# Performance work log

Hardware: AMD Instinct MI355X
Metric: run time of the kernel (lower is better)

Reference implementation:

```python
import jax, jax.numpy as jnp
import numpy as np

T, B, D, A = 512, 64, 1024, 128
NL = 2
AIN = A + 2 * D        # adapt LSTM input size: adapt + x + alstm hidden
PSZ = 2 * D + 12 * D   # policy size per layer (bias=True): ninp+nhid + 12*nhid


def setup_inputs() -> dict:
    key = jax.random.key(0)
    ks = jax.random.split(key, 12)
    r = lambda k, s: jax.random.normal(k, s, dtype=jnp.float32) * 0.03
    return {
        "x": jax.random.normal(ks[0], (T, B, D), dtype=jnp.float32),
        # layer 0
        "a_wih0": r(ks[1], (4 * A, AIN)), "a_whh0": r(ks[2], (4 * A, A)),
        "a_bih0": jnp.zeros((4 * A,), jnp.float32), "a_bhh0": jnp.zeros((4 * A,), jnp.float32),
        "p_w0": r(ks[3], (PSZ, A)), "p_b0": jnp.ones((PSZ,), jnp.float32),
        "f_wih0": r(ks[4], (4 * D, D)), "f_whh0": r(ks[5], (4 * D, D)),
        "f_b0": jnp.zeros((4 * D,), jnp.float32),
        # layer 1
        "a_wih1": r(ks[6], (4 * A, AIN)), "a_whh1": r(ks[7], (4 * A, A)),
        "a_bih1": jnp.zeros((4 * A,), jnp.float32), "a_bhh1": jnp.zeros((4 * A,), jnp.float32),
        "p_w1": r(ks[8], (PSZ, A)), "p_b1": jnp.ones((PSZ,), jnp.float32),
        "f_wih1": r(ks[9], (4 * D, D)), "f_whh1": r(ks[10], (4 * D, D)),
        "f_b1": jnp.zeros((4 * D,), jnp.float32),
    }


def _lstm_cell(x, h, c, wih, whh, bih, bhh):
    g = x @ wih.T + bih + h @ whh.T + bhh      # [B, 4A]
    i, f, gg, o = jnp.split(g, 4, axis=1)
    c2 = jax.nn.sigmoid(f) * c + jax.nn.sigmoid(i) * jnp.tanh(gg)
    h2 = jax.nn.sigmoid(o) * jnp.tanh(c2)
    return h2, c2


def _alstm_cell(xt, h, c, pol, wih, whh, b):
    # policy chunks: [ninp, nhid, 4n, 4n, 4n] with ninp=nhid=D
    p0 = pol[:, :D]
    p1 = pol[:, D:2 * D]
    p2 = pol[:, 2 * D:6 * D]
    p3 = pol[:, 6 * D:10 * D]
    p4 = pol[:, 10 * D:14 * D]
    ig = ((xt * p0) @ wih.T) * p2 + b * p4
    hg = ((h * p1) @ whh.T) * p3
    g = ig + hg
    i, f, gg, o = jnp.split(g, 4, axis=1)
    c2 = jax.nn.sigmoid(f) * c + jax.nn.sigmoid(i) * jnp.tanh(gg)
    h2 = jax.nn.sigmoid(o) * jnp.tanh(c2)
    return h2, c2


def reference(x, a_wih0, a_whh0, a_bih0, a_bhh0, p_w0, p_b0, f_wih0, f_whh0, f_b0,
              a_wih1, a_whh1, a_bih1, a_bhh1, p_w1, p_b1, f_wih1, f_whh1, f_b1):
    params = [
        (a_wih0, a_whh0, a_bih0, a_bhh0, p_w0, p_b0, f_wih0, f_whh0, f_b0),
        (a_wih1, a_whh1, a_bih1, a_bhh1, p_w1, p_b1, f_wih1, f_whh1, f_b1),
    ]

    def step(carry, xt):
        ah, ac, fh, fc = (list(t) for t in carry)
        xc = xt
        for l in range(NL):
            awih, awhh, abih, abhh, pw, pb, fwih, fwhh, fb = params[l]
            # nlayers != 1: adapt input = [x, alstm hidden, prev-layer adapt hidden]
            # (Python negative indexing at l=0 picks last layer's adapt hidden from t-1,
            #  matching the torch in-place list update semantics.)
            ax = jnp.concatenate([xc, fh[l], ah[l - 1]], axis=1)
            ah[l], ac[l] = _lstm_cell(ax, ah[l], ac[l], awih, awhh, abih, abhh)
            pol = ah[l] @ pw.T + pb                      # Project: Linear(A -> PSZ)
            fh[l], fc[l] = _alstm_cell(xc, fh[l], fc[l], pol, fwih, fwhh, fb)
            xc = fh[l]
        return (tuple(ah), tuple(ac), tuple(fh), tuple(fc)), xc

    za = jnp.zeros((B, A), x.dtype)
    zf = jnp.zeros((B, D), x.dtype)
    carry0 = ((za,) * NL, (za,) * NL, (zf,) * NL, (zf,) * NL)
    _, ys = jax.lax.scan(step, carry0, x)   # [T, B, D]
    return ys
```

## Files before the change

kernel.cpp:

```cpp
#include <hip/hip_runtime.h>

#define T_ 512
#define B_ 64
#define D_ 1024
#define A_ 128
#define KCAT_ 2304
#define PSZ_ 14336
#define NBLK 224

typedef __attribute__((ext_vector_type(8))) short short8;
typedef __attribute__((ext_vector_type(4))) short short4_t;
typedef __attribute__((ext_vector_type(4))) float float4_t;
typedef __attribute__((ext_vector_type(2))) unsigned long long ull2;

__device__ __forceinline__ float sigf(float x){ return 1.0f/(1.0f + __expf(-x)); }
__device__ __forceinline__ float tanhf_(float x){ return 2.0f/(1.0f + __expf(-2.0f*x)) - 1.0f; }

__device__ __forceinline__ short f2bf(float f){
  unsigned u = __builtin_bit_cast(unsigned, f);
  u += 0x7fffu + ((u >> 16) & 1u);
  return (short)(u >> 16);
}
__device__ __forceinline__ float bf2f(short s){
  unsigned u = ((unsigned)(unsigned short)s) << 16;
  return __builtin_bit_cast(float, u);
}

__device__ __forceinline__ unsigned ld_u32_cg(const void* p){
  return __hip_atomic_load((const unsigned*)p, __ATOMIC_RELAXED, __HIP_MEMORY_SCOPE_AGENT);
}
__device__ __forceinline__ unsigned long long ld_u64_cg(const void* p){
  return __hip_atomic_load((const unsigned long long*)p, __ATOMIC_RELAXED, __HIP_MEMORY_SCOPE_AGENT);
}
__device__ __forceinline__ void st_u32_cg(void* p, unsigned v){
  __hip_atomic_store((unsigned*)p, v, __ATOMIC_RELAXED, __HIP_MEMORY_SCOPE_AGENT);
}
__device__ __forceinline__ void st_u64_cg(void* p, unsigned long long v){
  __hip_atomic_store((unsigned long long*)p, v, __ATOMIC_RELAXED, __HIP_MEMORY_SCOPE_AGENT);
}
__device__ __forceinline__ float ld_f_cg(const float* p){
  unsigned u = ld_u32_cg(p); return __builtin_bit_cast(float, u);
}
__device__ __forceinline__ void st_f_cg(float* p, float v){
  st_u32_cg(p, __builtin_bit_cast(unsigned, v));
}
__device__ __forceinline__ short8 ld_bf8_cg(const short* p){
  ull2 t; t.x = ld_u64_cg(p); t.y = ld_u64_cg(p + 4);
  return __builtin_bit_cast(short8, t);
}
__device__ __forceinline__ short4_t ld_bf4_cg(const short* p){
  return __builtin_bit_cast(short4_t, ld_u64_cg(p));
}
__device__ __forceinline__ float4_t ld_f4_cg(const float* p){
  ull2 t; t.x = ld_u64_cg(p); t.y = ld_u64_cg(p + 2);
  return __builtin_bit_cast(float4_t, t);
}
__device__ __forceinline__ void st_bf4_cg(short* p, short4_t v){
  st_u64_cg(p, __builtin_bit_cast(unsigned long long, v));
}
__device__ __forceinline__ void st_f4_cg(float* p, float4_t v){
  ull2 t = __builtin_bit_cast(ull2, v);
  st_u64_cg(p, t.x); st_u64_cg(p + 2, t.y);
}

__global__ __launch_bounds__(256) void pk_cat(const float* __restrict__ wih,
                                              const float* __restrict__ whh,
                                              short* __restrict__ dst){
  int c = blockIdx.x*256 + threadIdx.x;
  int n = blockIdx.y;
  if (c >= KCAT_) return;
  float v = (c < 2176) ? wih[(size_t)n*2176 + c] : whh[n*A_ + (c - 2176)];
  dst[(size_t)n*KCAT_ + c] = f2bf(v);
}
__global__ __launch_bounds__(256) void pk_conv(const float* __restrict__ src,
                                               short* __restrict__ dst, int n){
  int i = blockIdx.x*256 + threadIdx.x;
  if (i < n) dst[i] = f2bf(src[i]);
}

struct Args {
  const float* x;
  const short* Wcat0; const short* Wcat1;
  const float* bih0;  const float* bih1;
  const float* bhh0;  const float* bhh1;
  const short* pw0;   const short* pw1;
  const float* pb0;   const float* pb1;
  const short* fwi0;  const short* fwi1;
  const short* fwh0;  const short* fwh1;
  const float* fb0;   const float* fb1;
  float* gates; float* ac; float* fc; float* polp;
  short* xp0; short* hp1; short* fhbf; short* ahbf;
  float* out;
  unsigned* bar;
};

__device__ __forceinline__ void gsync(unsigned* bar, unsigned target){
  __syncthreads();
  if (threadIdx.x == 0){
    __hip_atomic_fetch_add(bar, 1u, __ATOMIC_RELAXED, __HIP_MEMORY_SCOPE_AGENT);
    while (__hip_atomic_load(bar, __ATOMIC_RELAXED, __HIP_MEMORY_SCOPE_AGENT) < target)
      __builtin_amdgcn_s_sleep(2);
  }
  __syncthreads();
}

__global__ __launch_bounds__(256, 1) void fused(Args P){
  const int tid  = threadIdx.x;
  const int blk  = blockIdx.x;
  const int wq   = tid >> 6;
  const int lane = tid & 63;
  const int row  = lane & 15, quad = lane >> 4;

  __shared__ float red[4][256];
  __shared__ short ah_s[64*136];

  unsigned ph = 0;

  for (int t = 0; t < T_; ++t){
    const int par = t & 1, cur = par ^ 1;
    const float* xt = P.x + (size_t)t*B_*D_;
    #pragma unroll
    for (int l = 0; l < 2; ++l){
      const short* Wcat = l ? P.Wcat1 : P.Wcat0;
      const float* bih  = l ? P.bih1  : P.bih0;
      const float* bhh  = l ? P.bhh1  : P.bhh0;
      const short* pw   = l ? P.pw1   : P.pw0;
      const float* pb   = l ? P.pb1   : P.pb0;
      const short* fwi  = l ? P.fwi1  : P.fwi0;
      const short* fwh  = l ? P.fwh1  : P.fwh0;
      const float* fb   = l ? P.fb1   : P.fb0;
      short* fh_l = P.fhbf + (size_t)l*B_*D_;
      const short* ahp = l ? (P.ahbf + (0*2 + cur)*B_*A_)
                           : (P.ahbf + (1*2 + par)*B_*A_);
      const short* ahs = P.ahbf + (l*2 + par)*B_*A_;
      short* ah_out    = P.ahbf + (l*2 + cur)*B_*A_;
      const float* ac_old = P.ac + (l*2 + par)*A_*B_;
      float* ac_new       = P.ac + (l*2 + cur)*A_*B_;
      float* fc_l = P.fc + (size_t)l*B_*D_;

      if (blk < 128){
        const int m0  = (blk >> 2) * 16;
        const int nt1 = blk & 3;
        const int bq  = nt1*16 + row;
        const short* wrow = Wcat + (size_t)(m0 + row)*KCAT_ + quad*8;
        float4_t acc = {0.f,0.f,0.f,0.f};
        if (l == 0){
          const float* xp = xt + (size_t)bq*D_ + quad*8;
          #pragma unroll
          for (int i = 0; i < 8; ++i){
            const int ks = wq + 4*i;
            short8 a = *(const short8*)(wrow + ks*32);
            float4_t x0 = *(const float4_t*)(xp + ks*32);
            float4_t x1 = *(const float4_t*)(xp + ks*32 + 4);
            short8 bfr;
            #pragma unroll
            for (int r = 0; r < 4; ++r){ bfr[r] = f2bf(x0[r]); bfr[4+r] = f2bf(x1[r]); }
            acc = __builtin_amdgcn_mfma_f32_16x16x32_bf16(a, bfr, acc, 0, 0, 0);
          }
        } else {
          const short* xp = P.fhbf + (size_t)bq*D_;
          #pragma unroll
          for (int i = 0; i < 8; ++i){
            const int ks = wq + 4*i;
            short8 a = *(const short8*)(wrow + ks*32);
            short8 bfr = ld_bf8_cg(xp + quad*8 + ks*32);
            acc = __builtin_amdgcn_mfma_f32_16x16x32_bf16(a, bfr, acc, 0, 0, 0);
          }
        }
        {
          const short* hp = fh_l + (size_t)bq*D_;
          #pragma unroll
          for (int i = 0; i < 8; ++i){
            const int ks = wq + 4*i;
            short8 a = *(const short8*)(wrow + 1024 + ks*32);
            short8 bfr = ld_bf8_cg(hp + quad*8 + ks*32);
            acc = __builtin_amdgcn_mfma_f32_16x16x32_bf16(a, bfr, acc, 0, 0, 0);
          }
        }
        {
          short8 a = *(const short8*)(wrow + 2048 + wq*32);
          short8 bfr = ld_bf8_cg(ahp + bq*A_ + quad*8 + wq*32);
          acc = __builtin_amdgcn_mfma_f32_16x16x32_bf16(a, bfr, acc, 0, 0, 0);
        }
        {
          short8 a = *(const short8*)(wrow + 2176 + wq*32);
          short8 bfr = ld_bf8_cg(ahs + bq*A_ + quad*8 + wq*32);
          acc = __builtin_amdgcn_mfma_f32_16x16x32_bf16(a, bfr, acc, 0, 0, 0);
        }
        #pragma unroll
        for (int r = 0; r < 4; ++r) red[wq][(r << 6) | lane] = acc[r];
        __syncthreads();
        {
          float s = red[0][tid] + red[1][tid] + red[2][tid] + red[3][tid];
          const int rr = tid >> 6, ll = tid & 63;
          const int n = m0 + ((ll >> 4) << 2) + rr;
          const int b = nt1*16 + (ll & 15);
          st_f_cg(&P.gates[n*B_ + b], s + bih[n] + bhh[n]);
        }
      }
      gsync(P.bar, ++ph * NBLK);

      {
        const int b = tid & 63, q = tid >> 6;
        unsigned long long pk = 0;
        #pragma unroll 8
        for (int jj = 0; jj < 32; ++jj){
          const int j = q*32 + jj;
          float gi = ld_f_cg(&P.gates[(j      )*B_ + b]);
          float gf = ld_f_cg(&P.gates[(j + 128)*B_ + b]);
          float gg = ld_f_cg(&P.gates[(j + 256)*B_ + b]);
          float go = ld_f_cg(&P.gates[(j + 384)*B_ + b]);
          float c  = ld_f_cg(&ac_old[j*B_ + b]);
          float c2 = sigf(gf)*c + sigf(gi)*tanhf_(gg);
          float h2 = sigf(go)*tanhf_(c2);
          short hb = f2bf(h2);
          ah_s[b*136 + j] = hb;
          if (blk == 0){
            st_f_cg(&ac_new[j*B_ + b], c2);
            pk |= (unsigned long long)(unsigned short)hb << ((jj & 3)*16);
            if ((jj & 3) == 3){ st_u64_cg(ah_out + b*A_ + (j - 3), pk); pk = 0; }
          }
        }
        __syncthreads();
        const int m0 = (blk*4 + wq)*16;
        const short* wrow = pw + (size_t)(m0 + row)*A_ + quad*8;
        float4_t acc[4] = {{0.f,0.f,0.f,0.f},{0.f,0.f,0.f,0.f},{0.f,0.f,0.f,0.f},{0.f,0.f,0.f,0.f}};
        #pragma unroll
        for (int ks = 0; ks < 4; ++ks){
          short8 a = *(const short8*)(wrow + ks*32);
          #pragma unroll
          for (int nt = 0; nt < 4; ++nt){
            short8 bf8 = *(const short8*)&ah_s[(nt*16 + row)*136 + ks*32 + quad*8];
            acc[nt] = __builtin_amdgcn_mfma_f32_16x16x32_bf16(a, bf8, acc[nt], 0, 0, 0);
          }
        }
        const int c0 = m0 + quad*4;
        float4_t pbv = *(const float4_t*)(pb + c0);
        if (m0 < 1024){
          #pragma unroll
          for (int nt = 0; nt < 4; ++nt){
            const int b2 = nt*16 + row;
            float4_t xv;
            if (l == 0){ xv = *(const float4_t*)(xt + (size_t)b2*D_ + c0); }
            else {
              short4_t xb = ld_bf4_cg(P.fhbf + (size_t)b2*D_ + c0);
              #pragma unroll
              for (int r = 0; r < 4; ++r) xv[r] = bf2f(xb[r]);
            }
            short4_t o;
            #pragma unroll
            for (int r = 0; r < 4; ++r) o[r] = f2bf((acc[nt][r] + pbv[r]) * xv[r]);
            st_bf4_cg(P.xp0 + (size_t)b2*D_ + c0, o);
          }
        } else if (m0 < 2048){
          const int cc = c0 - 1024;
          #pragma unroll
          for (int nt = 0; nt < 4; ++nt){
            const int b2 = nt*16 + row;
            short4_t hb = ld_bf4_cg(fh_l + (size_t)b2*D_ + cc);
            short4_t o;
            #pragma unroll
            for (int r = 0; r < 4; ++r) o[r] = f2bf((acc[nt][r] + pbv[r]) * bf2f(hb[r]));
            st_bf4_cg(P.hp1 + (size_t)b2*D_ + cc, o);
          }
        } else {
          const int cc = c0 - 2048;
          #pragma unroll
          for (int nt = 0; nt < 4; ++nt){
            const int b2 = nt*16 + row;
            float4_t vv;
            #pragma unroll
            for (int r = 0; r < 4; ++r) vv[r] = acc[nt][r] + pbv[r];
            st_f4_cg(P.polp + (size_t)b2*12288 + cc, vv);
          }
        }
      }
      gsync(P.bar, ++ph * NBLK);

      if (blk < 64){
        const int nt3 = wq;
        const int j0 = blk*16;
        const short* wIr[4]; const short* wHr[4];
        #pragma unroll
        for (int g = 0; g < 4; ++g){
          wIr[g] = fwi + (size_t)(g*D_ + j0 + row)*D_ + quad*8;
          wHr[g] = fwh + (size_t)(g*D_ + j0 + row)*D_ + quad*8;
        }
        const short* bx = P.xp0 + (size_t)(nt3*16 + row)*D_ + quad*8;
        const short* bh = P.hp1 + (size_t)(nt3*16 + row)*D_ + quad*8;
        float4_t aI[4] = {{0.f,0.f,0.f,0.f},{0.f,0.f,0.f,0.f},{0.f,0.f,0.f,0.f},{0.f,0.f,0.f,0.f}};
        float4_t aH[4] = {{0.f,0.f,0.f,0.f},{0.f,0.f,0.f,0.f},{0.f,0.f,0.f,0.f},{0.f,0.f,0.f,0.f}};
        #pragma unroll 2
        for (int ks = 0; ks < 32; ++ks){
          const int kg = ks*32;
          short8 bxf = ld_bf8_cg(bx + kg);
          short8 bhf = ld_bf8_cg(bh + kg);
          #pragma unroll
          for (int g = 0; g < 4; ++g){
            short8 ai  = *(const short8*)(wIr[g] + kg);
            short8 ah8 = *(const short8*)(wHr[g] + kg);
            aI[g] = __builtin_amdgcn_mfma_f32_16x16x32_bf16(ai,  bxf, aI[g], 0, 0, 0);
            aH[g] = __builtin_amdgcn_mfma_f32_16x16x32_bf16(ah8, bhf, aH[g], 0, 0, 0);
          }
        }
        const int b3 = nt3*16 + row;
        const int jr = j0 + quad*4;
        float4_t gl[4];
        #pragma unroll
        for (int g = 0; g < 4; ++g){
          const float* pbase = P.polp + (size_t)b3*12288 + g*D_ + jr;
          float4_t p2 = ld_f4_cg(pbase);
          float4_t p3 = ld_f4_cg(pbase + 4096);
          float4_t p4 = ld_f4_cg(pbase + 8192);
          float4_t fbv = *(const float4_t*)(fb + g*D_ + jr);
          #pragma unroll
          for (int r = 0; r < 4; ++r)
            gl[g][r] = aI[g][r]*p2[r] + fbv[r]*p4[r] + aH[g][r]*p3[r];
        }
        float4_t cold = *(const float4_t*)(fc_l + (size_t)b3*D_ + jr);
        float4_t cnew, hnew;
        #pragma unroll
        for (int r = 0; r < 4; ++r){
          float c2 = sigf(gl[1][r])*cold[r] + sigf(gl[0][r])*tanhf_(gl[2][r]);
          float h2 = sigf(gl[3][r])*tanhf_(c2);
          cnew[r] = c2; hnew[r] = h2;
        }
        *(float4_t*)(fc_l + (size_t)b3*D_ + jr) = cnew;
        short4_t hb;
        #pragma unroll
        for (int r = 0; r < 4; ++r) hb[r] = f2bf(hnew[r]);
        st_bf4_cg(fh_l + (size_t)b3*D_ + jr, hb);
        if (l == 1)
          __builtin_nontemporal_store(hnew,
              (float4_t*)(P.out + (size_t)t*B_*D_ + (size_t)b3*D_ + jr));
      }
      gsync(P.bar, ++ph * NBLK);
    }
  }
}

extern "C" void kernel_launch(void* const* d_in, const int* in_sizes, int n_in,
                              void* d_out, int out_size, void* d_ws, size_t ws_size,
                              hipStream_t stream) {
  const float* x = (const float*)d_in[0];
  const float* a_wih[2] = {(const float*)d_in[1],  (const float*)d_in[10]};
  const float* a_whh[2] = {(const float*)d_in[2],  (const float*)d_in[11]};
  const float* a_bih[2] = {(const float*)d_in[3],  (const float*)d_in[12]};
  const float* a_bhh[2] = {(const float*)d_in[4],  (const float*)d_in[13]};
  const float* p_w[2]   = {(const float*)d_in[5],  (const float*)d_in[14]};
  const float* p_b[2]   = {(const float*)d_in[6],  (const float*)d_in[15]};
  const float* f_wih[2] = {(const float*)d_in[7],  (const float*)d_in[16]};
  const float* f_whh[2] = {(const float*)d_in[8],  (const float*)d_in[17]};
  const float* f_b[2]   = {(const float*)d_in[9],  (const float*)d_in[18]};

  char* w = (char*)d_ws;
  float* gates = (float*)(w + 0);
  float* ac    = (float*)(w + 131072);
  float* fc    = (float*)(w + 262144);
  float* polp  = (float*)(w + 786432);
  short* xp0   = (short*)(w + 3932160);
  short* hp1   = (short*)(w + 4063232);
  short* fhbf  = (short*)(w + 4194304);
  short* ahbf  = (short*)(w + 4456448);
  short* Wcat  = (short*)(w + 4521984);
  short* pwbf  = (short*)(w + 9240576);
  short* fwihb = (short*)(w + 16580608);
  short* fwhhb = (short*)(w + 33357824);
  unsigned* bar = (unsigned*)(w + 50135040);

  hipMemsetAsync(w + 131072, 0, 655360, stream);
  hipMemsetAsync(w + 4194304, 0, 327680, stream);
  hipMemsetAsync(w + 50135040, 0, 64, stream);

  for (int l = 0; l < 2; ++l){
    pk_cat<<<dim3(9,512), 256, 0, stream>>>(a_wih[l], a_whh[l], Wcat + (size_t)l*512*KCAT_);
    pk_conv<<<(PSZ_*A_ + 255)/256, 256, 0, stream>>>(p_w[l], pwbf + (size_t)l*PSZ_*A_, PSZ_*A_);
    pk_conv<<<(4*D_*D_ + 255)/256, 256, 0, stream>>>(f_wih[l], fwihb + (size_t)l*4*D_*D_, 4*D_*D_);
    pk_conv<<<(4*D_*D_ + 255)/256, 256, 0, stream>>>(f_whh[l], fwhhb + (size_t)l*4*D_*D_, 4*D_*D_);
  }

  Args A;
  A.x = x;
  A.Wcat0 = Wcat;  A.Wcat1 = Wcat + (size_t)512*KCAT_;
  A.bih0 = a_bih[0]; A.bih1 = a_bih[1];
  A.bhh0 = a_bhh[0]; A.bhh1 = a_bhh[1];
  A.pw0 = pwbf;    A.pw1 = pwbf + (size_t)PSZ_*A_;
  A.pb0 = p_b[0];  A.pb1 = p_b[1];
  A.fwi0 = fwihb;  A.fwi1 = fwihb + (size_t)4*D_*D_;
  A.fwh0 = fwhhb;  A.fwh1 = fwhhb + (size_t)4*D_*D_;
  A.fb0 = f_b[0];  A.fb1 = f_b[1];
  A.gates = gates; A.ac = ac; A.fc = fc; A.polp = polp;
  A.xp0 = xp0; A.hp1 = hp1; A.fhbf = fhbf; A.ahbf = ahbf;
  A.out = (float*)d_out;
  A.bar = bar;

  fused<<<NBLK, 256, 0, stream>>>(A);
}
```

Before: 96.72 ms.

## Keep ALSTM weights resident in LDS across all timesteps with flag-based grid barrier

The persistent kernel now uses 256 blocks. Each block converts its slice of the adaptive-LSTM input and hidden weights to bf16 once and keeps them in shared memory for the whole sequence, so it no longer streams them from global memory every step. Each layer's gate GEMM runs on the 128 blocks that own that layer's slice, with a lane shuffle to combine the gates. The atomic-counter barrier becomes per-block flags that every block polls, and the small adapt-LSTM GEMM moves to 32 blocks with no cross-wave reduction. In exchange, half the blocks sit idle in the ALSTM phase of each layer, and about 132KB of LDS per block limits occupancy to one block per CU.

```diff
diff --git a/kernel.cpp b/kernel.cpp
--- a/kernel.cpp
+++ b/kernel.cpp
@@ -6,7 +6,8 @@
 #define A_ 128
 #define KCAT_ 2304
 #define PSZ_ 14336
-#define NBLK 224
+#define NBLK 256
+#define RS_ 1032
 
 typedef __attribute__((ext_vector_type(8))) short short8;
 typedef __attribute__((ext_vector_type(4))) short short4_t;
@@ -85,24 +86,14 @@
   const float* bhh0;  const float* bhh1;
   const short* pw0;   const short* pw1;
   const float* pb0;   const float* pb1;
-  const short* fwi0;  const short* fwi1;
-  const short* fwh0;  const short* fwh1;
+  const float* fwi32_0; const float* fwi32_1;
+  const float* fwh32_0; const float* fwh32_1;
   const float* fb0;   const float* fb1;
   float* gates; float* ac; float* fc; float* polp;
   short* xp0; short* hp1; short* fhbf; short* ahbf;
   float* out;
-  unsigned* bar;
+  unsigned* flags;
 };
-
-__device__ __forceinline__ void gsync(unsigned* bar, unsigned target){
-  __syncthreads();
-  if (threadIdx.x == 0){
-    __hip_atomic_fetch_add(bar, 1u, __ATOMIC_RELAXED, __HIP_MEMORY_SCOPE_AGENT);
-    while (__hip_atomic_load(bar, __ATOMIC_RELAXED, __HIP_MEMORY_SCOPE_AGENT) < target)
-      __builtin_amdgcn_s_sleep(2);
-  }
-  __syncthreads();
-}
 
 __global__ __launch_bounds__(256, 1) void fused(Args P){
   const int tid  = threadIdx.x;
@@ -111,8 +102,28 @@
   const int lane = tid & 63;
   const int row  = lane & 15, quad = lane >> 4;
 
-  __shared__ float red[4][256];
+  __shared__ short wlds[2][32][RS_];
   __shared__ short ah_s[64*136];
+
+  {
+    const int l3 = blk >> 7, jt = blk & 127;
+    const float* srcI = l3 ? P.fwi32_1 : P.fwi32_0;
+    const float* srcH = l3 ? P.fwh32_1 : P.fwh32_0;
+    for (int e = tid; e < 8192; e += 256){
+      const int rr = e >> 8;
+      const int k4 = (e & 255) << 2;
+      const int g = rr >> 3, r = rr & 7;
+      const size_t off = ((size_t)(g*1024 + jt*8 + r))*1024 + k4;
+      float4_t vI = *(const float4_t*)(srcI + off);
+      float4_t vH = *(const float4_t*)(srcH + off);
+      short4_t oI, oH;
+      #pragma unroll
+      for (int j = 0; j < 4; ++j){ oI[j] = f2bf(vI[j]); oH[j] = f2bf(vH[j]); }
+      *(short4_t*)&wlds[0][rr][k4] = oI;
+      *(short4_t*)&wlds[1][rr][k4] = oH;
+    }
+    __syncthreads();
+  }
 
   unsigned ph = 0;
 
@@ -126,8 +137,6 @@
       const float* bhh  = l ? P.bhh1  : P.bhh0;
       const short* pw   = l ? P.pw1   : P.pw0;
       const float* pb   = l ? P.pb1   : P.pb0;
-      const short* fwi  = l ? P.fwi1  : P.fwi0;
-      const short* fwh  = l ? P.fwh1  : P.fwh0;
       const float* fb   = l ? P.fb1   : P.fb0;
       short* fh_l = P.fhbf + (size_t)l*B_*D_;
       const short* ahp = l ? (P.ahbf + (0*2 + cur)*B_*A_)
@@ -138,17 +147,15 @@
       float* ac_new       = P.ac + (l*2 + cur)*A_*B_;
       float* fc_l = P.fc + (size_t)l*B_*D_;
 
-      if (blk < 128){
-        const int m0  = (blk >> 2) * 16;
-        const int nt1 = blk & 3;
-        const int bq  = nt1*16 + row;
+      if (blk < 32){
+        const int m0 = blk*16;
+        const int bq = wq*16 + row;
         const short* wrow = Wcat + (size_t)(m0 + row)*KCAT_ + quad*8;
         float4_t acc = {0.f,0.f,0.f,0.f};
         if (l == 0){
           const float* xp = xt + (size_t)bq*D_ + quad*8;
-          #pragma unroll
-          for (int i = 0; i < 8; ++i){
-            const int ks = wq + 4*i;
+          #pragma unroll 4
+          for (int ks = 0; ks < 32; ++ks){
             short8 a = *(const short8*)(wrow + ks*32);
             float4_t x0 = *(const float4_t*)(xp + ks*32);
             float4_t x1 = *(const float4_t*)(xp + ks*32 + 4);
@@ -158,49 +165,53 @@
             acc = __builtin_amdgcn_mfma_f32_16x16x32_bf16(a, bfr, acc, 0, 0, 0);
           }
         } else {
-          const short* xp = P.fhbf + (size_t)bq*D_;
-          #pragma unroll
-          for (int i = 0; i < 8; ++i){
-            const int ks = wq + 4*i;
+          const short* xp = P.fhbf + (size_t)bq*D_ + quad*8;
+          #pragma unroll 4
+          for (int ks = 0; ks < 32; ++ks){
             short8 a = *(const short8*)(wrow + ks*32);
-            short8 bfr = ld_bf8_cg(xp + quad*8 + ks*32);
+            short8 bfr = ld_bf8_cg(xp + ks*32);
             acc = __builtin_amdgcn_mfma_f32_16x16x32_bf16(a, bfr, acc, 0, 0, 0);
           }
         }
         {
-          const short* hp = fh_l + (size_t)bq*D_;
-          #pragma unroll
-          for (int i = 0; i < 8; ++i){
-            const int ks = wq + 4*i;
+          const short* hp = fh_l + (size_t)bq*D_ + quad*8;
+          #pragma unroll 4
+          for (int ks = 0; ks < 32; ++ks){
             short8 a = *(const short8*)(wrow + 1024 + ks*32);
-            short8 bfr = ld_bf8_cg(hp + quad*8 + ks*32);
+            short8 bfr = ld_bf8_cg(hp + ks*32);
             acc = __builtin_amdgcn_mfma_f32_16x16x32_bf16(a, bfr, acc, 0, 0, 0);
           }
         }
-        {
-          short8 a = *(const short8*)(wrow + 2048 + wq*32);
-          short8 bfr = ld_bf8_cg(ahp + bq*A_ + quad*8 + wq*32);
+        #pragma unroll
+        for (int ks = 0; ks < 4; ++ks){
+          short8 a = *(const short8*)(wrow + 2048 + ks*32);
+          short8 bfr = ld_bf8_cg(ahp + bq*A_ + quad*8 + ks*32);
           acc = __builtin_amdgcn_mfma_f32_16x16x32_bf16(a, bfr, acc, 0, 0, 0);
         }
-        {
-          short8 a = *(const short8*)(wrow + 2176 + wq*32);
-          short8 bfr = ld_bf8_cg(ahs + bq*A_ + quad*8 + wq*32);
+        #pragma unroll
+        for (int ks = 0; ks < 4; ++ks){
+          short8 a = *(const short8*)(wrow + 2176 + ks*32);
+          short8 bfr = ld_bf8_cg(ahs + bq*A_ + quad*8 + ks*32);
           acc = __builtin_amdgcn_mfma_f32_16x16x32_bf16(a, bfr, acc, 0, 0, 0);
         }
         #pragma unroll
-        for (int r = 0; r < 4; ++r) red[wq][(r << 6) | lane] = acc[r];
+        for (int r = 0; r < 4; ++r){
+          const int n = m0 + quad*4 + r;
+          st_f_cg(&P.gates[n*B_ + bq], acc[r] + bih[n] + bhh[n]);
+        }
+      }
+      {
+        ++ph;
         __syncthreads();
-        {
-          float s = red[0][tid] + red[1][tid] + red[2][tid] + red[3][tid];
-          const int rr = tid >> 6, ll = tid & 63;
-          const int n = m0 + ((ll >> 4) << 2) + rr;
-          const int b = nt1*16 + (ll & 15);
-          st_f_cg(&P.gates[n*B_ + b], s + bih[n] + bhh[n]);
-        }
-      }
-      gsync(P.bar, ++ph * NBLK);
-
-      {
+        if (tid == 0) st_u32_cg(P.flags + blk*16, ph);
+        for (;;){
+          int bad = (ld_u32_cg(P.flags + tid*16) < ph);
+          if (__syncthreads_count(bad) == 0) break;
+          __builtin_amdgcn_s_sleep(1);
+        }
+      }
+
+      if (blk < 224){
         const int b = tid & 63, q = tid >> 6;
         unsigned long long pk = 0;
         #pragma unroll 8
@@ -275,66 +286,87 @@
           }
         }
       }
-      gsync(P.bar, ++ph * NBLK);
-
-      if (blk < 64){
-        const int nt3 = wq;
-        const int j0 = blk*16;
-        const short* wIr[4]; const short* wHr[4];
-        #pragma unroll
-        for (int g = 0; g < 4; ++g){
-          wIr[g] = fwi + (size_t)(g*D_ + j0 + row)*D_ + quad*8;
-          wHr[g] = fwh + (size_t)(g*D_ + j0 + row)*D_ + quad*8;
-        }
-        const short* bx = P.xp0 + (size_t)(nt3*16 + row)*D_ + quad*8;
-        const short* bh = P.hp1 + (size_t)(nt3*16 + row)*D_ + quad*8;
-        float4_t aI[4] = {{0.f,0.f,0.f,0.f},{0.f,0.f,0.f,0.f},{0.f,0.f,0.f,0.f},{0.f,0.f,0.f,0.f}};
-        float4_t aH[4] = {{0.f,0.f,0.f,0.f},{0.f,0.f,0.f,0.f},{0.f,0.f,0.f,0.f},{0.f,0.f,0.f,0.f}};
+      {
+        ++ph;
+        __syncthreads();
+        if (tid == 0) st_u32_cg(P.flags + blk*16, ph);
+        for (;;){
+          int bad = (ld_u32_cg(P.flags + tid*16) < ph);
+          if (__syncthreads_count(bad) == 0) break;
+          __builtin_amdgcn_s_sleep(1);
+        }
+      }
+
+      if ((blk >> 7) == l){
+        const int jt = blk & 127;
+        const int b  = wq*16 + row;
+        const short* bx = P.xp0 + (size_t)b*D_ + quad*8;
+        const short* bh = P.hp1 + (size_t)b*D_ + quad*8;
+        float4_t aI[2] = {{0.f,0.f,0.f,0.f},{0.f,0.f,0.f,0.f}};
+        float4_t aH[2] = {{0.f,0.f,0.f,0.f},{0.f,0.f,0.f,0.f}};
         #pragma unroll 2
         for (int ks = 0; ks < 32; ++ks){
-          const int kg = ks*32;
-          short8 bxf = ld_bf8_cg(bx + kg);
-          short8 bhf = ld_bf8_cg(bh + kg);
-          #pragma unroll
-          for (int g = 0; g < 4; ++g){
-            short8 ai  = *(const short8*)(wIr[g] + kg);
-            short8 ah8 = *(const short8*)(wHr[g] + kg);
-            aI[g] = __builtin_amdgcn_mfma_f32_16x16x32_bf16(ai,  bxf, aI[g], 0, 0, 0);
-            aH[g] = __builtin_amdgcn_mfma_f32_16x16x32_bf16(ah8, bhf, aH[g], 0, 0, 0);
-          }
-        }
-        const int b3 = nt3*16 + row;
-        const int jr = j0 + quad*4;
-        float4_t gl[4];
-        #pragma unroll
-        for (int g = 0; g < 4; ++g){
-          const float* pbase = P.polp + (size_t)b3*12288 + g*D_ + jr;
+          short8 bxf = ld_bf8_cg(bx + ks*32);
+          short8 bhf = ld_bf8_cg(bh + ks*32);
+          #pragma unroll
+          for (int tp = 0; tp < 2; ++tp){
+            short8 aIf = *(const short8*)&wlds[0][tp*16 + row][quad*8 + ks*32];
+            short8 aHf = *(const short8*)&wlds[1][tp*16 + row][quad*8 + ks*32];
+            aI[tp] = __builtin_amdgcn_mfma_f32_16x16x32_bf16(aIf, bxf, aI[tp], 0, 0, 0);
+            aH[tp] = __builtin_amdgcn_mfma_f32_16x16x32_bf16(aHf, bhf, aH[tp], 0, 0, 0);
+          }
+        }
+        const int g0 = quad >> 1;
+        const int jb = (quad & 1) * 4;
+        const int jg = jt*8 + jb;
+        float gl[2][4];
+        #pragma unroll
+        for (int tp = 0; tp < 2; ++tp){
+          const int g = tp*2 + g0;
+          const float* pbase = P.polp + (size_t)b*12288 + g*1024 + jg;
           float4_t p2 = ld_f4_cg(pbase);
           float4_t p3 = ld_f4_cg(pbase + 4096);
           float4_t p4 = ld_f4_cg(pbase + 8192);
-          float4_t fbv = *(const float4_t*)(fb + g*D_ + jr);
+          float4_t fbv = *(const float4_t*)(fb + g*1024 + jg);
           #pragma unroll
           for (int r = 0; r < 4; ++r)
-            gl[g][r] = aI[g][r]*p2[r] + fbv[r]*p4[r] + aH[g][r]*p3[r];
-        }
-        float4_t cold = *(const float4_t*)(fc_l + (size_t)b3*D_ + jr);
-        float4_t cnew, hnew;
-        #pragma unroll
-        for (int r = 0; r < 4; ++r){
-          float c2 = sigf(gl[1][r])*cold[r] + sigf(gl[0][r])*tanhf_(gl[2][r]);
-          float h2 = sigf(gl[3][r])*tanhf_(c2);
-          cnew[r] = c2; hnew[r] = h2;
-        }
-        *(float4_t*)(fc_l + (size_t)b3*D_ + jr) = cnew;
-        short4_t hb;
-        #pragma unroll
-        for (int r = 0; r < 4; ++r) hb[r] = f2bf(hnew[r]);
-        st_bf4_cg(fh_l + (size_t)b3*D_ + jr, hb);
-        if (l == 1)
-          __builtin_nontemporal_store(hnew,
-              (float4_t*)(P.out + (size_t)t*B_*D_ + (size_t)b3*D_ + jr));
-      }
-      gsync(P.bar, ++ph * NBLK);
+            gl[tp][r] = aI[tp][r]*p2[r] + aH[tp][r]*p3[r] + fbv[r]*p4[r];
+        }
+        float glx[2][4];
+        #pragma unroll
+        for (int tp = 0; tp < 2; ++tp)
+          #pragma unroll
+          for (int r = 0; r < 4; ++r)
+            glx[tp][r] = __shfl_xor(gl[tp][r], 32, 64);
+        if (quad < 2){
+          float4_t cold = *(const float4_t*)(fc_l + (size_t)b*D_ + jg);
+          float4_t cnew, hnew;
+          #pragma unroll
+          for (int r = 0; r < 4; ++r){
+            float c2 = sigf(glx[0][r])*cold[r] + sigf(gl[0][r])*tanhf_(gl[1][r]);
+            float h2 = sigf(glx[1][r])*tanhf_(c2);
+            cnew[r] = c2; hnew[r] = h2;
+          }
+          *(float4_t*)(fc_l + (size_t)b*D_ + jg) = cnew;
+          short4_t hb;
+          #pragma unroll
+          for (int r = 0; r < 4; ++r) hb[r] = f2bf(hnew[r]);
+          st_bf4_cg(fh_l + (size_t)b*D_ + jg, hb);
+          if (l == 1)
+            __builtin_nontemporal_store(hnew,
+                (float4_t*)(P.out + (size_t)t*B_*D_ + (size_t)b*D_ + jg));
+        }
+      }
+      {
+        ++ph;
+        __syncthreads();
+        if (tid == 0) st_u32_cg(P.flags + blk*16, ph);
+        for (;;){
+          int bad = (ld_u32_cg(P.flags + tid*16) < ph);
+          if (__syncthreads_count(bad) == 0) break;
+          __builtin_amdgcn_s_sleep(1);
+        }
+      }
     }
   }
 }
@@ -364,19 +396,15 @@
   short* ahbf  = (short*)(w + 4456448);
   short* Wcat  = (short*)(w + 4521984);
   short* pwbf  = (short*)(w + 9240576);
-  short* fwihb = (short*)(w + 16580608);
-  short* fwhhb = (short*)(w + 33357824);
-  unsigned* bar = (unsigned*)(w + 50135040);
+  unsigned* flags = (unsigned*)(w + 16580608);
 
   hipMemsetAsync(w + 131072, 0, 655360, stream);
   hipMemsetAsync(w + 4194304, 0, 327680, stream);
-  hipMemsetAsync(w + 50135040, 0, 64, stream);
+  hipMemsetAsync(w + 16580608, 0, 16384, stream);
 
   for (int l = 0; l < 2; ++l){
     pk_cat<<<dim3(9,512), 256, 0, stream>>>(a_wih[l], a_whh[l], Wcat + (size_t)l*512*KCAT_);
     pk_conv<<<(PSZ_*A_ + 255)/256, 256, 0, stream>>>(p_w[l], pwbf + (size_t)l*PSZ_*A_, PSZ_*A_);
-    pk_conv<<<(4*D_*D_ + 255)/256, 256, 0, stream>>>(f_wih[l], fwihb + (size_t)l*4*D_*D_, 4*D_*D_);
-    pk_conv<<<(4*D_*D_ + 255)/256, 256, 0, stream>>>(f_whh[l], fwhhb + (size_t)l*4*D_*D_, 4*D_*D_);
   }
 
   Args A;
@@ -386,13 +414,13 @@
   A.bhh0 = a_bhh[0]; A.bhh1 = a_bhh[1];
   A.pw0 = pwbf;    A.pw1 = pwbf + (size_t)PSZ_*A_;
   A.pb0 = p_b[0];  A.pb1 = p_b[1];
-  A.fwi0 = fwihb;  A.fwi1 = fwihb + (size_t)4*D_*D_;
-  A.fwh0 = fwhhb;  A.fwh1 = fwhhb + (size_t)4*D_*D_;
+  A.fwi32_0 = f_wih[0]; A.fwi32_1 = f_wih[1];
+  A.fwh32_0 = f_whh[0]; A.fwh32_1 = f_whh[1];
   A.fb0 = f_b[0];  A.fb1 = f_b[1];
   A.gates = gates; A.ac = ac; A.fc = fc; A.polp = polp;
   A.xp0 = xp0; A.hp1 = hp1; A.fhbf = fhbf; A.ahbf = ahbf;
   A.out = (float*)d_out;
-  A.bar = bar;
+  A.flags = flags;
 
   fused<<<NBLK, 256, 0, stream>>>(A);
 }
```

Measured after the change: 81.75 ms. 15.5% less time.
